# Kernel optimization log

Hardware: AMD Instinct MI355X
Metric: run time of the kernel (lower is better)

## Reference

```python
import jax, jax.numpy as jnp
import numpy as np

B, T, N, H = 512, 128, 256, 256  # batch, time_step, input_size, hidden_size


def setup_inputs() -> dict:
    key = jax.random.key(0)
    ks = jax.random.split(key, 8)
    s_lin = 1.0 / np.sqrt(T)
    s_ih = 1.0 / np.sqrt(H)
    return {
        "X": jax.random.normal(ks[0], (B, T, N), dtype=jnp.float32),
        "Wq": jax.random.uniform(ks[1], (T, T), jnp.float32, -s_lin, s_lin),
        "Wk": jax.random.uniform(ks[2], (T, T), jnp.float32, -s_lin, s_lin),
        "Wv": jax.random.uniform(ks[3], (T, T), jnp.float32, -s_lin, s_lin),
        "W_ih": jax.random.uniform(ks[4], (4 * H, N), jnp.float32, -s_ih, s_ih),
        "W_hh": jax.random.uniform(ks[5], (4 * H, H), jnp.float32, -s_ih, s_ih),
        "b_ih": jax.random.uniform(ks[6], (4 * H,), jnp.float32, -s_ih, s_ih),
        "b_hh": jax.random.uniform(ks[7], (4 * H,), jnp.float32, -s_ih, s_ih),
    }


def _forward(X, Wq, Wk, Wv, W_ih, W_hh, b_ih, b_hh):
    b, t, n = X.shape
    Xp = jnp.swapaxes(X, 1, 2)  # (B, N, T)
    Q = Xp @ Wq.T               # (B, N, T)
    K = Xp @ Wk.T               # (B, N, T)
    V = Xp @ Wv.T               # (B, N, T)
    # QK[b,i,j] = sum_t Q[b,i,t] * K[b,j,t]; scale by sqrt(N)
    scores = jnp.einsum('bit,bjt->bij', Q, K) / jnp.sqrt(jnp.float32(n))
    A = jax.nn.softmax(scores, axis=-1)          # (B, N, N)
    Xa = jnp.einsum('bij,bjt->bit', A, V)        # (B, N, T)
    Xa = jnp.swapaxes(Xa, 1, 2)                  # (B, T, N)

    h0 = jnp.zeros((b, W_hh.shape[1]), X.dtype)
    c0 = h0

    def step(carry, x_t):
        h, c = carry
        gates = x_t @ W_ih.T + b_ih + h @ W_hh.T + b_hh  # (B, 4H)
        i, f, g, o = jnp.split(gates, 4, axis=-1)         # PyTorch gate order
        i = jax.nn.sigmoid(i)
        f = jax.nn.sigmoid(f)
        g = jnp.tanh(g)
        o = jax.nn.sigmoid(o)
        c = f * c + i * g
        h = o * jnp.tanh(c)
        return (h, c), h

    _, hs = jax.lax.scan(step, (h0, c0), jnp.swapaxes(Xa, 0, 1))  # (T, B, H)
    return jnp.swapaxes(hs, 0, 1)  # (B, T, H)


def reference(X, Wq, Wk, Wv, W_ih, W_hh, b_ih, b_hh):
    return _forward(X, Wq, Wk, Wv, W_ih, W_hh, b_ih, b_hh)
```

## Files before the change

kernel.cpp:

```cpp
#include <hip/hip_runtime.h>
#include <hip/hip_bf16.h>
#include <stdint.h>


#define DI __device__ __forceinline__

typedef __attribute__((ext_vector_type(8))) short bf16x8;
typedef __attribute__((ext_vector_type(4))) short short4v;
typedef __attribute__((ext_vector_type(4))) float f32x4;
typedef __attribute__((ext_vector_type(4))) int int4v;

union U8 { bf16x8 v; short4v h[2]; int4v i; };

DI unsigned short f2bf(float x){
  union { float f; unsigned u; } v; v.f = x;
  unsigned r = v.u + 0x7fffu + ((v.u >> 16) & 1u);
  return (unsigned short)(r >> 16);
}
DI float bf2f(unsigned short x){
  union { unsigned u; float f; } v; v.u = ((unsigned)x) << 16; return v.f;
}
DI float rcp_(float x){ return __builtin_amdgcn_rcpf(x); }
DI float sigm(float x){ return rcp_(1.0f + __expf(-x)); }
DI float tanhf_(float x){ return 1.0f - 2.0f * rcp_(1.0f + __expf(2.0f * x)); }

#define BB 512
#define TT 128
#define NN 256
#define HH 256

__global__ void k_prep(const float* __restrict__ Wq, const float* __restrict__ Wk,
                       const float* __restrict__ Wv,
                       const float* __restrict__ bih, const float* __restrict__ bhh,
                       unsigned short* __restrict__ wqb, unsigned short* __restrict__ wkb,
                       unsigned short* __restrict__ wvb,
                       float* __restrict__ bias, int* __restrict__ flags){
  int i = blockIdx.x * 256 + threadIdx.x;
  if (i < 16384){ wqb[i] = f2bf(Wq[i]); wkb[i] = f2bf(Wk[i]); wvb[i] = f2bf(Wv[i]); }
  if (i < 1024){ bias[i] = bih[i] + bhh[i]; }
  if (i < 256){ flags[i] = 0; }
}

__global__ void k_prep2(const float* __restrict__ W, unsigned short* __restrict__ w_f){
  int idx = blockIdx.x * 256 + threadIdx.x;
  int j = idx >> 3, kk = idx & 7;
  const float* src = W + j * 256 + kk * 32;
  unsigned short o[32];
  #pragma unroll
  for (int g = 0; g < 4; ++g)
    #pragma unroll
    for (int e = 0; e < 4; ++e){
      o[g * 8 + e]     = f2bf(src[4 * g + e]);
      o[g * 8 + 4 + e] = f2bf(src[16 + 4 * g + e]);
    }
  int4v* dst = (int4v*)((char*)w_f + j * 512 + kk * 64);
  #pragma unroll
  for (int q = 0; q < 4; ++q) dst[q] = *(int4v*)(o + q * 8);
}

__global__ __launch_bounds__(256) void k_xpose(const float* __restrict__ X,
                                               unsigned short* __restrict__ Xp){
  __shared__ float tile[128][65];
  int b = blockIdx.y, n0 = blockIdx.x * 64;
  int tid = threadIdx.x;
  int nloc = tid & 63, t0 = tid >> 6;
  const float* src = X + (size_t)b * TT * NN + n0 + nloc;
  #pragma unroll
  for (int r = 0; r < 32; ++r){
    int t = r * 4 + t0;
    tile[t][nloc] = src[(size_t)t * NN];
  }
  __syncthreads();
  int tl = tid & 127, nr0 = tid >> 7;
  unsigned short* dst = Xp + ((size_t)b * NN + n0) * TT + tl;
  #pragma unroll
  for (int r = 0; r < 32; ++r){
    int n = r * 2 + nr0;
    dst[(size_t)n * TT] = f2bf(tile[tl][n]);
  }
}

__global__ __launch_bounds__(256) void k_qkv(const unsigned short* __restrict__ Xp,
      const unsigned short* __restrict__ Wqb, const unsigned short* __restrict__ Wkb,
      const unsigned short* __restrict__ Wvb,
      unsigned short* __restrict__ Qo, unsigned short* __restrict__ Ko,
      unsigned short* __restrict__ Vo){
  __shared__ __align__(16) char smem[32768 + 8192];
  unsigned short* Bs = (unsigned short*)smem;
  char* As = smem + 32768;
  char* Os = smem;
  int mode = blockIdx.y;
  const unsigned short* W = (mode == 0) ? Wqb : ((mode == 1) ? Wkb : Wvb);
  int m0 = blockIdx.x * 128;
  int tid = threadIdx.x;

  #pragma unroll
  for (int it = 0; it < 16; ++it){
    int c = it * 256 + tid;
    int j = c >> 5;
    int kc = (c & 31) << 2;
    short4v v = *(const short4v*)(W + j * 128 + kc);
    *(short4v*)((char*)Bs + j * 256 + ((kc * 2) ^ ((j & 7) << 4))) = v;
  }

  int lane = tid & 63, wv = tid >> 6;
  int wr = wv >> 1, wc = wv & 1;
  int l15 = lane & 15, g = lane >> 4;
  f32x4 zro = {0.f, 0.f, 0.f, 0.f};
  f32x4 acc[4][4];
  #pragma unroll
  for (int a = 0; a < 4; ++a)
    #pragma unroll
    for (int bq = 0; bq < 4; ++bq) acc[a][bq] = zro;

  int arow = tid >> 1, ahalf = (tid & 1) * 16;
  const unsigned short* Ap = Xp + (size_t)(m0 + arow) * 128;

  for (int ks = 0; ks < 4; ++ks){
    __syncthreads();
    {
      const unsigned short* s = Ap + ks * 32 + ahalf;
      char* base = As + arow * 64;
      int kb = ahalf * 2;
      int sw = (arow & 7) << 3;
      *(short4v*)(base + ((kb     ) ^ sw)) = *(const short4v*)(s);
      *(short4v*)(base + ((kb +  8) ^ sw)) = *(const short4v*)(s + 4);
      *(short4v*)(base + ((kb + 16) ^ sw)) = *(const short4v*)(s + 8);
      *(short4v*)(base + ((kb + 24) ^ sw)) = *(const short4v*)(s + 12);
    }
    __syncthreads();
    U8 af[4];
    #pragma unroll
    for (int mt = 0; mt < 4; ++mt){
      int ar = wr * 64 + mt * 16 + l15;
      const char* ab = As + ar * 64;
      int sw = (ar & 7) << 3;
      af[mt].h[0] = *(const short4v*)(ab + ((8 * g) ^ sw));
      af[mt].h[1] = *(const short4v*)(ab + ((8 * g + 32) ^ sw));
    }
    #pragma unroll
    for (int nt = 0; nt < 4; ++nt){
      int jr = wc * 64 + nt * 16 + l15;
      const char* bb = (const char*)Bs + jr * 256;
      int kb = ks * 64 + 8 * g, sw = (jr & 7) << 4;
      U8 bf;
      bf.h[0] = *(const short4v*)(bb + (kb ^ sw));
      bf.h[1] = *(const short4v*)(bb + ((kb + 32) ^ sw));
      #pragma unroll
      for (int mt = 0; mt < 4; ++mt)
        acc[mt][nt] = __builtin_amdgcn_mfma_f32_16x16x32_bf16(af[mt].v, bf.v, acc[mt][nt], 0, 0, 0);
    }
  }
  __syncthreads();
  float scale = (mode == 0) ? 0.0625f : 1.0f;
  #pragma unroll
  for (int mt = 0; mt < 4; ++mt)
    #pragma unroll
    for (int nt = 0; nt < 4; ++nt)
      #pragma unroll
      for (int r = 0; r < 4; ++r){
        int row = wr * 64 + mt * 16 + g * 4 + r;
        int col = wc * 64 + nt * 16 + l15;
        unsigned short hv = f2bf(acc[mt][nt][r] * scale);
        int addr = (mode == 2) ? (col * 256 + ((row * 2) ^ ((col & 7) << 4)))
                               : (row * 256 + ((col * 2) ^ ((row & 7) << 4)));
        *(unsigned short*)(Os + addr) = hv;
      }
  __syncthreads();
  int orow = tid >> 1, oseg = tid & 1;
  const char* srcrow = Os + orow * 256;
  unsigned short* dst;
  if (mode == 2){
    int bq = m0 >> 8, ibase = m0 & 255;
    dst = Vo + ((size_t)bq * 128 + orow) * 256 + ibase + oseg * 64;
  } else {
    dst = ((mode == 0) ? Qo : Ko) + (size_t)(m0 + orow) * 128 + oseg * 64;
  }
  #pragma unroll
  for (int c = 0; c < 8; ++c){
    int kb = oseg * 128 + c * 16;
    *(int4v*)((char*)dst + c * 16) = *(const int4v*)(srcrow + (kb ^ ((orow & 7) << 4)));
  }
}

__global__ __launch_bounds__(256) void k_attn(const unsigned short* __restrict__ Q,
        const unsigned short* __restrict__ K, const unsigned short* __restrict__ Vt,
        unsigned short* __restrict__ Xa){
  __shared__ __align__(16) char smem[16384 + 65536 + 32768 + 256];
  char* Qs = smem;
  char* Ks = smem + 16384;
  char* Ps = smem + 16384 + 65536;
  float* rden = (float*)(smem + 16384 + 65536 + 32768);
  int b = blockIdx.y, i0 = blockIdx.x * 64;
  int tid = threadIdx.x, lane = tid & 63, wv = tid >> 6;
  int l15 = lane & 15, g = lane >> 4;

  {
    int row = tid >> 2, q = tid & 3;
    const char* src = (const char*)(Q + ((size_t)b * 256 + i0 + row) * 128) + q * 64;
    char* dstr = Qs + row * 256;
    int sw = (row & 7) << 4;
    #pragma unroll
    for (int c = 0; c < 4; ++c){
      int kb = q * 64 + c * 16;
      *(int4v*)(dstr + (kb ^ sw)) = *(const int4v*)(src + c * 16);
    }
  }
  {
    const char* src = (const char*)(K + ((size_t)b * 256 + tid) * 128);
    char* dstr = Ks + tid * 256;
    int sw = (tid & 7) << 4;
    #pragma unroll
    for (int c = 0; c < 16; ++c)
      *(int4v*)(dstr + ((c * 16) ^ sw)) = *(const int4v*)(src + c * 16);
  }
  __syncthreads();

  f32x4 zro = {0.f, 0.f, 0.f, 0.f};
  f32x4 acc[16];
  #pragma unroll
  for (int nt = 0; nt < 16; ++nt) acc[nt] = zro;
  #pragma unroll
  for (int kk = 0; kk < 4; ++kk){
    int ar = wv * 16 + l15;
    const char* ab = Qs + ar * 256;
    int kb = kk * 64 + 8 * g, swa = (ar & 7) << 4;
    U8 a;
    a.h[0] = *(const short4v*)(ab + (kb ^ swa));
    a.h[1] = *(const short4v*)(ab + ((kb + 32) ^ swa));
    #pragma unroll
    for (int nt = 0; nt < 16; ++nt){
      int jr = nt * 16 + l15;
      const char* bb = Ks + jr * 256;
      int swb = (jr & 7) << 4;
      U8 bf;
      bf.h[0] = *(const short4v*)(bb + (kb ^ swb));
      bf.h[1] = *(const short4v*)(bb + ((kb + 32) ^ swb));
      acc[nt] = __builtin_amdgcn_mfma_f32_16x16x32_bf16(a.v, bf.v, acc[nt], 0, 0, 0);
    }
  }
  float mx[4], sm[4];
  #pragma unroll
  for (int r = 0; r < 4; ++r){
    float m = acc[0][r];
    #pragma unroll
    for (int nt = 1; nt < 16; ++nt) m = fmaxf(m, acc[nt][r]);
    #pragma unroll
    for (int s = 1; s < 16; s <<= 1) m = fmaxf(m, __shfl_xor(m, s));
    mx[r] = m;
  }
  #pragma unroll
  for (int r = 0; r < 4; ++r){
    float s = 0.f;
    #pragma unroll
    for (int nt = 0; nt < 16; ++nt){
      float p = __expf(acc[nt][r] - mx[r]);
      acc[nt][r] = p; s += p;
    }
    #pragma unroll
    for (int sd = 1; sd < 16; sd <<= 1) s += __shfl_xor(s, sd);
    sm[r] = s;
  }
  #pragma unroll
  for (int nt = 0; nt < 16; ++nt)
    #pragma unroll
    for (int r = 0; r < 4; ++r){
      int ir = wv * 16 + g * 4 + r;
      *(unsigned short*)(Ps + ir * 512 + ((nt * 16 + l15) * 2 ^ ((ir & 7) << 4))) = f2bf(acc[nt][r]);
    }
  #pragma unroll
  for (int r = 0; r < 4; ++r)
    if (l15 == r) rden[wv * 16 + g * 4 + r] = rcp_(sm[r]);
  __syncthreads();
  {
    int row = tid >> 1, half = tid & 1;
    const char* src = (const char*)(Vt + ((size_t)b * 128 + row) * 256) + half * 256;
    char* dstr = Ks + row * 512;
    int sw = (row & 7) << 4;
    #pragma unroll
    for (int c = 0; c < 16; ++c){
      int jb = half * 256 + c * 16;
      *(int4v*)(dstr + (jb ^ sw)) = *(const int4v*)(src + c * 16);
    }
  }
  __syncthreads();

  f32x4 acc2[2][4];
  #pragma unroll
  for (int mt = 0; mt < 2; ++mt)
    #pragma unroll
    for (int nt = 0; nt < 4; ++nt) acc2[mt][nt] = zro;
  #pragma unroll
  for (int kk = 0; kk < 8; ++kk){
    int kb = kk * 64 + 8 * g;
    U8 bfr[4];
    #pragma unroll
    for (int nt = 0; nt < 4; ++nt){
      int ir = nt * 16 + l15;
      const char* pb = Ps + ir * 512;
      int sw = (ir & 7) << 4;
      bfr[nt].h[0] = *(const short4v*)(pb + (kb ^ sw));
      bfr[nt].h[1] = *(const short4v*)(pb + ((kb + 32) ^ sw));
    }
    #pragma unroll
    for (int mt = 0; mt < 2; ++mt){
      int tr = wv * 32 + mt * 16 + l15;
      const char* ab = Ks + tr * 512;
      int sw = (tr & 7) << 4;
      U8 a;
      a.h[0] = *(const short4v*)(ab + (kb ^ sw));
      a.h[1] = *(const short4v*)(ab + ((kb + 32) ^ sw));
      #pragma unroll
      for (int nt = 0; nt < 4; ++nt)
        acc2[mt][nt] = __builtin_amdgcn_mfma_f32_16x16x32_bf16(a.v, bfr[nt].v, acc2[mt][nt], 0, 0, 0);
    }
  }
  #pragma unroll
  for (int nt = 0; nt < 4; ++nt){
    float rd = rden[nt * 16 + l15];
    #pragma unroll
    for (int mt = 0; mt < 2; ++mt)
      #pragma unroll
      for (int r = 0; r < 4; ++r){
        int t = wv * 32 + mt * 16 + g * 4 + r;
        int i = i0 + nt * 16 + l15;
        Xa[((size_t)b * 128 + t) * 256 + i] = f2bf(acc2[mt][nt][r] * rd);
      }
  }
}

__global__ __launch_bounds__(512, 2) void k_lstm7(const unsigned short* __restrict__ Xa,
        const unsigned short* __restrict__ whh_f, const unsigned short* __restrict__ wih_f,
        const float* __restrict__ bias, float* __restrict__ out,
        unsigned int* __restrict__ hbuf, int* __restrict__ flags){
  __shared__ __align__(16) char smem[131072 + 8192 + 8192 + 8448];
  char* WI = smem;
  char* HS = smem + 131072;
  char* XS = smem + 139264;
  float* GS = (float*)(smem + 147456);
  int tid = threadIdx.x, lane = tid & 63, wv = tid >> 6;
  int l15 = lane & 15, g = lane >> 4;
  int bid = blockIdx.x;
  int x = bid & 7, q = bid >> 3;
  int y = q >> 2, m = q & 3;
  int grp = y * 8 + x;
  int b0 = grp * 8;
  int c0 = m * 64;
  int tb = tid >> 6, tc = tid & 63;

  U8 breg[2][8];
  #pragma unroll
  for (int nt = 0; nt < 2; ++nt){
    int jl = wv * 32 + nt * 16 + l15;
    int jg = (jl >> 6) * 256 + c0 + (jl & 63);
    #pragma unroll
    for (int kk = 0; kk < 8; ++kk)
      breg[nt][kk].i = *(const int4v*)((const char*)whh_f + (size_t)jg * 512 + kk * 64 + g * 16);
  }
  {
    int jl = tid >> 1, hq = (tid & 1) * 16;
    int jg = (jl >> 6) * 256 + c0 + (jl & 63);
    const char* src = (const char*)wih_f + (size_t)jg * 512;
    char* dst = WI + jl * 512;
    int sx = jl & 7;
    #pragma unroll
    for (int c2 = 0; c2 < 16; ++c2){
      int c = hq + c2;
      *(int4v*)(dst + ((c ^ sx) << 4)) = *(const int4v*)(src + c * 16);
    }
  }
  { int4v z = {0,0,0,0}; *(int4v*)(HS + tid * 16) = z; }
  if (tid < 256){ int4v z = {0,0,0,0}; *(int4v*)(XS + 4096 + tid * 16) = z; }
  {
    short4v v = *(const short4v*)(Xa + ((size_t)(b0 + tb) * 128) * 256 + tc * 4);
    *(short4v*)(XS + tb * 512 + ((tc * 8) ^ ((tb & 7) << 3))) = v;
  }
  float bs0 = bias[      c0 + tc], bs1 = bias[256 + c0 + tc];
  float bs2 = bias[512 + c0 + tc], bs3 = bias[768 + c0 + tc];
  float cst = 0.f;
  __syncthreads();

  int swA = (l15 & 7) << 3;
  const char* hsrow = HS + l15 * 512;
  const char* xsrow = XS + l15 * 512;
  const char* wib0 = WI + (wv * 32 + l15) * 512;
  const char* wib1 = WI + (wv * 32 + 16 + l15) * 512;
  int keep = g >> 1;
  #pragma unroll 1
  for (int t = 0; t < 128; ++t){
    f32x4 zro = {0.f, 0.f, 0.f, 0.f};
    f32x4 acc[2] = {zro, zro};
    #pragma unroll
    for (int kk = 0; kk < 8; ++kk){
      U8 a, a2, w0, w1;
      a.h[0]  = *(const short4v*)(hsrow + ((kk * 64 + 8 * g) ^ swA));
      a.h[1]  = *(const short4v*)(hsrow + ((kk * 64 + 32 + 8 * g) ^ swA));
      a2.h[0] = *(const short4v*)(xsrow + ((kk * 64 + 8 * g) ^ swA));
      a2.h[1] = *(const short4v*)(xsrow + ((kk * 64 + 32 + 8 * g) ^ swA));
      int cx = ((kk * 4 + g) ^ (l15 & 7)) << 4;
      w0.i = *(const int4v*)(wib0 + cx);
      w1.i = *(const int4v*)(wib1 + cx);
      acc[0] = __builtin_amdgcn_mfma_f32_16x16x32_bf16(a.v,  breg[0][kk].v, acc[0], 0, 0, 0);
      acc[1] = __builtin_amdgcn_mfma_f32_16x16x32_bf16(a.v,  breg[1][kk].v, acc[1], 0, 0, 0);
      acc[0] = __builtin_amdgcn_mfma_f32_16x16x32_bf16(a2.v, w0.v,          acc[0], 0, 0, 0);
      acc[1] = __builtin_amdgcn_mfma_f32_16x16x32_bf16(a2.v, w1.v,          acc[1], 0, 0, 0);
    }
    #pragma unroll
    for (int r = 0; r < 4; ++r){
      float v0 = acc[0][r], v1 = acc[1][r];
      float kv = keep ? v1 : v0;
      float sv = keep ? v0 : v1;
      float val = kv + __shfl_xor(sv, 32);
      int jl = wv * 32 + keep * 16 + l15;
      int batch = (g & 1) * 4 + r;
      GS[batch * 264 + (jl >> 6) * 66 + (jl & 63)] = val;
    }
    __syncthreads();
    float gv0 = GS[tb * 264 +   0 + tc];
    float gv1 = GS[tb * 264 +  66 + tc];
    float gv2 = GS[tb * 264 + 132 + tc];
    float gv3 = GS[tb * 264 + 198 + tc];
    short4v xan = {0, 0, 0, 0};
    if (t < 127)
      xan = *(const short4v*)(Xa + ((size_t)(b0 + tb) * 128 + (t + 1)) * 256 + tc * 4);
    float gi = sigm(gv0 + bs0);
    float gf = sigm(gv1 + bs1);
    float gg = tanhf_(gv2 + bs2);
    float go = sigm(gv3 + bs3);
    float c = gf * cst + gi * gg;
    cst = c;
    float h = go * tanhf_(c);
    out[((size_t)(b0 + tb) * 128 + t) * 256 + c0 + tc] = h;
    if (t < 127){
      unsigned short hhi = f2bf(h);
      unsigned short hlo = f2bf(h - bf2f(hhi));
      unsigned int pk = (unsigned int)hhi | ((unsigned int)hlo << 16);
      unsigned int* hb = hbuf + ((size_t)grp * 2 + (t & 1)) * 2048;
      __hip_atomic_store(hb + tb * 256 + c0 + tc, pk, __ATOMIC_RELAXED, __HIP_MEMORY_SCOPE_SYSTEM);
      __syncthreads();
      if (wv == 0){
        if (lane == 0)
          __hip_atomic_store(&flags[grp * 4 + m], t + 1, __ATOMIC_RELAXED, __HIP_MEMORY_SCOPE_SYSTEM);
        if (lane >= 1 && lane <= 3){
          int pl = lane - 1;
          int pslot = pl + (pl >= m ? 1 : 0);
          while (__hip_atomic_load(&flags[grp * 4 + pslot], __ATOMIC_RELAXED,
                                   __HIP_MEMORY_SCOPE_SYSTEM) <= t){}
        }
      }
      __syncthreads();
      {
        int bb = tid >> 6, cg = tid & 63;
        const unsigned long long* sp =
            (const unsigned long long*)(hb + bb * 256 + cg * 4);
        unsigned long long w0 = __hip_atomic_load(sp,     __ATOMIC_RELAXED, __HIP_MEMORY_SCOPE_SYSTEM);
        unsigned long long w1 = __hip_atomic_load(sp + 1, __ATOMIC_RELAXED, __HIP_MEMORY_SCOPE_SYSTEM);
        unsigned int u0 = (unsigned int)w0, u1 = (unsigned int)(w0 >> 32);
        unsigned int u2 = (unsigned int)w1, u3 = (unsigned int)(w1 >> 32);
        short4v hiv = { (short)(u0 & 0xffff), (short)(u1 & 0xffff),
                        (short)(u2 & 0xffff), (short)(u3 & 0xffff) };
        short4v lov = { (short)(u0 >> 16), (short)(u1 >> 16),
                        (short)(u2 >> 16), (short)(u3 >> 16) };
        int sw = (bb & 7) << 3;
        int cb = (cg * 8) ^ sw;
        *(short4v*)(HS + bb * 512 + cb) = hiv;
        *(short4v*)(HS + (bb + 8) * 512 + cb) = lov;
        *(short4v*)(XS + bb * 512 + cb) = xan;
      }
      __syncthreads();
    }
  }
}

extern "C" void kernel_launch(void* const* d_in, const int* in_sizes, int n_in,
                              void* d_out, int out_size, void* d_ws, size_t ws_size,
                              hipStream_t stream){
  (void)in_sizes; (void)n_in; (void)out_size; (void)ws_size;
  const float* X   = (const float*)d_in[0];
  const float* Wq  = (const float*)d_in[1];
  const float* Wk  = (const float*)d_in[2];
  const float* Wv  = (const float*)d_in[3];
  const float* Wih = (const float*)d_in[4];
  const float* Whh = (const float*)d_in[5];
  const float* bih = (const float*)d_in[6];
  const float* bhh = (const float*)d_in[7];
  float* out = (float*)d_out;
  char* ws = (char*)d_ws;

  const size_t SZ = 33554432ULL;
  unsigned short* p_xp = (unsigned short*)ws;
  unsigned short* p_q  = (unsigned short*)(ws + SZ);
  unsigned short* p_k  = (unsigned short*)(ws + 2 * SZ);
  unsigned short* p_vt = (unsigned short*)(ws + 3 * SZ);
  unsigned short* p_xa = (unsigned short*)(ws + 4 * SZ);
  char* p = ws + 5 * SZ;
  unsigned short* p_wqb = (unsigned short*)p; p += 32768;
  unsigned short* p_wkb = (unsigned short*)p; p += 32768;
  unsigned short* p_wvb = (unsigned short*)p; p += 32768;
  unsigned short* p_whhf= (unsigned short*)p; p += 524288;
  unsigned short* p_wihf= (unsigned short*)p; p += 524288;
  float* p_bias = (float*)p; p += 4096;
  unsigned int* p_hbuf = (unsigned int*)p; p += 1048576;
  int* p_flags = (int*)p;

  k_prep<<<64, 256, 0, stream>>>(Wq, Wk, Wv, bih, bhh,
                                 p_wqb, p_wkb, p_wvb, p_bias, p_flags);
  k_prep2<<<32, 256, 0, stream>>>(Whh, p_whhf);
  k_prep2<<<32, 256, 0, stream>>>(Wih, p_wihf);
  k_xpose<<<dim3(4, 512), 256, 0, stream>>>(X, p_xp);
  k_qkv<<<dim3(1024, 3), 256, 0, stream>>>(p_xp, p_wqb, p_wkb, p_wvb, p_q, p_k, p_vt);
  k_attn<<<dim3(4, 512), 256, 0, stream>>>(p_q, p_k, p_vt, p_xa);
  k_lstm7<<<256, 512, 0, stream>>>(p_xa, p_whhf, p_wihf, p_bias, out, p_hbuf, p_flags);
}
```

Measured before the change: 611.1 us.

## Overlap next-step input projection MFMAs with cross-block flag spin-wait

Moves the x_t @ W_ih part of the LSTM gate computation out of the serial per-step critical path. It is now computed for step t+1 while the block waits on peer-block flags for the h exchange. The next Xa row is loaded at the start of each step and written into shared memory before the barrier, so its load latency is hidden as well. This shortens the dependent chain per time step but adds live accumulator registers and reorders the shared-memory writes to XS.

```diff
diff --git a/kernel.cpp b/kernel.cpp
--- a/kernel.cpp
+++ b/kernel.cpp
@@ -329,7 +329,7 @@
   }
 }
 
-__global__ __launch_bounds__(512, 2) void k_lstm7(const unsigned short* __restrict__ Xa,
+__global__ __launch_bounds__(512, 2) void k_lstm8(const unsigned short* __restrict__ Xa,
         const unsigned short* __restrict__ whh_f, const unsigned short* __restrict__ wih_f,
         const float* __restrict__ bias, float* __restrict__ out,
         unsigned int* __restrict__ hbuf, int* __restrict__ flags){
@@ -386,24 +386,34 @@
   const char* wib0 = WI + (wv * 32 + l15) * 512;
   const char* wib1 = WI + (wv * 32 + 16 + l15) * 512;
   int keep = g >> 1;
+  f32x4 zro = {0.f, 0.f, 0.f, 0.f};
+
+  f32x4 accX[2] = {zro, zro};
+  #pragma unroll
+  for (int kk = 0; kk < 8; ++kk){
+    U8 a2, w0, w1;
+    a2.h[0] = *(const short4v*)(xsrow + ((kk * 64 + 8 * g) ^ swA));
+    a2.h[1] = *(const short4v*)(xsrow + ((kk * 64 + 32 + 8 * g) ^ swA));
+    int cx = ((kk * 4 + g) ^ (l15 & 7)) << 4;
+    w0.i = *(const int4v*)(wib0 + cx);
+    w1.i = *(const int4v*)(wib1 + cx);
+    accX[0] = __builtin_amdgcn_mfma_f32_16x16x32_bf16(a2.v, w0.v, accX[0], 0, 0, 0);
+    accX[1] = __builtin_amdgcn_mfma_f32_16x16x32_bf16(a2.v, w1.v, accX[1], 0, 0, 0);
+  }
+
   #pragma unroll 1
   for (int t = 0; t < 128; ++t){
-    f32x4 zro = {0.f, 0.f, 0.f, 0.f};
-    f32x4 acc[2] = {zro, zro};
+    short4v xan = {0, 0, 0, 0};
+    if (t < 127)
+      xan = *(const short4v*)(Xa + ((size_t)(b0 + tb) * 128 + (t + 1)) * 256 + tc * 4);
+    f32x4 acc[2] = {accX[0], accX[1]};
     #pragma unroll
     for (int kk = 0; kk < 8; ++kk){
-      U8 a, a2, w0, w1;
-      a.h[0]  = *(const short4v*)(hsrow + ((kk * 64 + 8 * g) ^ swA));
-      a.h[1]  = *(const short4v*)(hsrow + ((kk * 64 + 32 + 8 * g) ^ swA));
-      a2.h[0] = *(const short4v*)(xsrow + ((kk * 64 + 8 * g) ^ swA));
-      a2.h[1] = *(const short4v*)(xsrow + ((kk * 64 + 32 + 8 * g) ^ swA));
-      int cx = ((kk * 4 + g) ^ (l15 & 7)) << 4;
-      w0.i = *(const int4v*)(wib0 + cx);
-      w1.i = *(const int4v*)(wib1 + cx);
-      acc[0] = __builtin_amdgcn_mfma_f32_16x16x32_bf16(a.v,  breg[0][kk].v, acc[0], 0, 0, 0);
-      acc[1] = __builtin_amdgcn_mfma_f32_16x16x32_bf16(a.v,  breg[1][kk].v, acc[1], 0, 0, 0);
-      acc[0] = __builtin_amdgcn_mfma_f32_16x16x32_bf16(a2.v, w0.v,          acc[0], 0, 0, 0);
-      acc[1] = __builtin_amdgcn_mfma_f32_16x16x32_bf16(a2.v, w1.v,          acc[1], 0, 0, 0);
+      U8 a;
+      a.h[0] = *(const short4v*)(hsrow + ((kk * 64 + 8 * g) ^ swA));
+      a.h[1] = *(const short4v*)(hsrow + ((kk * 64 + 32 + 8 * g) ^ swA));
+      acc[0] = __builtin_amdgcn_mfma_f32_16x16x32_bf16(a.v, breg[0][kk].v, acc[0], 0, 0, 0);
+      acc[1] = __builtin_amdgcn_mfma_f32_16x16x32_bf16(a.v, breg[1][kk].v, acc[1], 0, 0, 0);
     }
     #pragma unroll
     for (int r = 0; r < 4; ++r){
@@ -420,9 +430,6 @@
     float gv1 = GS[tb * 264 +  66 + tc];
     float gv2 = GS[tb * 264 + 132 + tc];
     float gv3 = GS[tb * 264 + 198 + tc];
-    short4v xan = {0, 0, 0, 0};
-    if (t < 127)
-      xan = *(const short4v*)(Xa + ((size_t)(b0 + tb) * 128 + (t + 1)) * 256 + tc * 4);
     float gi = sigm(gv0 + bs0);
     float gf = sigm(gv1 + bs1);
     float gg = tanhf_(gv2 + bs2);
@@ -437,16 +444,27 @@
       unsigned int pk = (unsigned int)hhi | ((unsigned int)hlo << 16);
       unsigned int* hb = hbuf + ((size_t)grp * 2 + (t & 1)) * 2048;
       __hip_atomic_store(hb + tb * 256 + c0 + tc, pk, __ATOMIC_RELAXED, __HIP_MEMORY_SCOPE_SYSTEM);
+      *(short4v*)(XS + tb * 512 + ((tc * 8) ^ ((tb & 7) << 3))) = xan;
       __syncthreads();
-      if (wv == 0){
-        if (lane == 0)
-          __hip_atomic_store(&flags[grp * 4 + m], t + 1, __ATOMIC_RELAXED, __HIP_MEMORY_SCOPE_SYSTEM);
-        if (lane >= 1 && lane <= 3){
-          int pl = lane - 1;
-          int pslot = pl + (pl >= m ? 1 : 0);
-          while (__hip_atomic_load(&flags[grp * 4 + pslot], __ATOMIC_RELAXED,
-                                   __HIP_MEMORY_SCOPE_SYSTEM) <= t){}
-        }
+      if (wv == 0 && lane == 0)
+        __hip_atomic_store(&flags[grp * 4 + m], t + 1, __ATOMIC_RELAXED, __HIP_MEMORY_SCOPE_SYSTEM);
+      accX[0] = zro; accX[1] = zro;
+      #pragma unroll
+      for (int kk = 0; kk < 8; ++kk){
+        U8 a2, w0, w1;
+        a2.h[0] = *(const short4v*)(xsrow + ((kk * 64 + 8 * g) ^ swA));
+        a2.h[1] = *(const short4v*)(xsrow + ((kk * 64 + 32 + 8 * g) ^ swA));
+        int cx = ((kk * 4 + g) ^ (l15 & 7)) << 4;
+        w0.i = *(const int4v*)(wib0 + cx);
+        w1.i = *(const int4v*)(wib1 + cx);
+        accX[0] = __builtin_amdgcn_mfma_f32_16x16x32_bf16(a2.v, w0.v, accX[0], 0, 0, 0);
+        accX[1] = __builtin_amdgcn_mfma_f32_16x16x32_bf16(a2.v, w1.v, accX[1], 0, 0, 0);
+      }
+      if (wv == 0 && lane >= 1 && lane <= 3){
+        int pl = lane - 1;
+        int pslot = pl + (pl >= m ? 1 : 0);
+        while (__hip_atomic_load(&flags[grp * 4 + pslot], __ATOMIC_RELAXED,
+                                 __HIP_MEMORY_SCOPE_SYSTEM) <= t){}
       }
       __syncthreads();
       {
@@ -465,7 +483,6 @@
         int cb = (cg * 8) ^ sw;
         *(short4v*)(HS + bb * 512 + cb) = hiv;
         *(short4v*)(HS + (bb + 8) * 512 + cb) = lov;
-        *(short4v*)(XS + bb * 512 + cb) = xan;
       }
       __syncthreads();
     }
@@ -510,5 +527,5 @@
   k_xpose<<<dim3(4, 512), 256, 0, stream>>>(X, p_xp);
   k_qkv<<<dim3(1024, 3), 256, 0, stream>>>(p_xp, p_wqb, p_wkb, p_wvb, p_q, p_k, p_vt);
   k_attn<<<dim3(4, 512), 256, 0, stream>>>(p_q, p_k, p_vt, p_xa);
-  k_lstm7<<<256, 512, 0, stream>>>(p_xa, p_whhf, p_wihf, p_bias, out, p_hbuf, p_flags);
-}
+  k_lstm8<<<256, 512, 0, stream>>>(p_xa, p_whhf, p_wihf, p_bias, out, p_hbuf, p_flags);
+}
```

Result: faster. 528.2 us (-13.6%).
